# Optimization experiments

Measured on AMD Instinct MI355X. Metric: run time of the kernel, lower is better.

Reference implementation:

```python
import jax, jax.numpy as jnp
import numpy as np

N_EMBD = 1024
HEAD_SIZE = N_EMBD  # source bug: Block passes n_embd as head_size
EPS = 1e-5

def layernorm(x, g, b):
    mu = jnp.mean(x, axis=-1, keepdims=True)
    var = jnp.var(x, axis=-1, keepdims=True)
    return (x - mu) * jax.lax.rsqrt(var + EPS) * g + b

def setup_inputs() -> dict:
    key = jax.random.key(0)
    ks = jax.random.split(key, 8)
    B, T, C = 4, 2048, N_EMBD
    s = lambda fan_in: 1.0 / np.sqrt(fan_in)
    return {
        "x": jax.random.normal(ks[0], (B, T, C), dtype=jnp.float32),
        "Wk": jax.random.uniform(ks[1], (C, HEAD_SIZE), jnp.float32, -s(C), s(C)),
        "Wq": jax.random.uniform(ks[2], (C, HEAD_SIZE), jnp.float32, -s(C), s(C)),
        "Wv": jax.random.uniform(ks[3], (C, HEAD_SIZE), jnp.float32, -s(C), s(C)),
        "W1": jax.random.uniform(ks[4], (C, 4 * C), jnp.float32, -s(C), s(C)),
        "b1": jnp.zeros((4 * C,), jnp.float32),
        "W2": jax.random.uniform(ks[5], (4 * C, C), jnp.float32, -s(4 * C), s(4 * C)),
        "b2": jnp.zeros((C,), jnp.float32),
        "g1": jnp.ones((C,), jnp.float32),
        "be1": jnp.zeros((C,), jnp.float32),
        "g2": jnp.ones((C,), jnp.float32),
        "be2": jnp.zeros((C,), jnp.float32),
    }

def reference(x, Wk, Wq, Wv, W1, b1, W2, b2, g1, be1, g2, be2):
    B, T, C = x.shape
    h = layernorm(x, g1, be1)
    q = h @ Wq              # [B,T,H]
    k = h @ Wk
    v = h @ Wv
    wei = jnp.einsum('bth,bsh->bts', q, k) / jnp.sqrt(jnp.float32(C))
    causal = jnp.tril(jnp.ones((T, T), dtype=bool))
    wei = jnp.where(causal, wei, -jnp.inf)
    wei = jax.nn.softmax(wei, axis=-1)
    sa = jnp.einsum('bts,bsh->bth', wei, v)
    x = x + sa
    h2 = layernorm(x, g2, be2)
    ff = jax.nn.relu(h2 @ W1 + b1) @ W2 + b2
    return x + ff
```

## Files before the change

### kernel.cpp

```cpp
#include <hip/hip_runtime.h>
#include <hip/hip_bf16.h>


typedef __bf16 bf16x8_t __attribute__((ext_vector_type(8)));
typedef float f32x4_t __attribute__((ext_vector_type(4)));

__device__ __forceinline__ unsigned short f2bf(float f) {
    unsigned int u = __float_as_uint(f);
    u += 0x7fffu + ((u >> 16) & 1u);
    return (unsigned short)(u >> 16);
}
__device__ __forceinline__ float bf2f(unsigned short u) {
    return __uint_as_float((unsigned int)u << 16);
}

__device__ __forceinline__ void gload16(const void* g, void* lds) {
    __builtin_amdgcn_global_load_lds(
        (const __attribute__((address_space(1))) unsigned int*)g,
        (__attribute__((address_space(3))) unsigned int*)lds, 16, 0, 0);
}

#define SB0() __builtin_amdgcn_sched_barrier(0)
#define BAR() asm volatile("s_barrier" ::: "memory")
#define VM4_BAR() asm volatile("s_waitcnt vmcnt(4)\ns_barrier" ::: "memory")
#define VM0_BAR() asm volatile("s_waitcnt vmcnt(0)\ns_barrier" ::: "memory")

enum { EPI_F32 = 0, EPI_BF16 = 1, EPI_BIAS_RELU_BF16 = 2, EPI_RESID_F32 = 3,
       EPI_BIAS_RESID_F32 = 4 };

template <int EPI, bool CSKIP, bool KLIM>
__global__ __launch_bounds__(512, 2) void gemm256(
    const unsigned short* __restrict__ A,
    const unsigned short* __restrict__ Bm,
    void* __restrict__ Cout,
    const float* __restrict__ bias,
    const float* __restrict__ resid,
    int M, int N, int K, int lda, int ldb, float scale,
    long long batA, long long batB, long long batC, long long batR)
{
    __shared__ __align__(16) unsigned char lds[131072];

    const int gx = gridDim.x;
    const int nwg = gx * gridDim.y;
    int bl = blockIdx.y * gx + blockIdx.x;
    bl = (bl & 7) * (nwg >> 3) + (bl >> 3);
    const int bx = bl % gx, by = bl / gx;

    const int row0 = by * 256, col0 = bx * 256;
    if (CSKIP && col0 > row0) return;

    const int bz = blockIdx.z;
    const unsigned short* Ab = A + (long long)bz * batA + (long long)row0 * lda;
    const unsigned short* Bb = Bm + (long long)bz * batB + (long long)col0 * ldb;

    const int tid = threadIdx.x, lane = tid & 63, wid = tid >> 6;
    const int wrM = (wid >> 2) * 128;
    const int wcN = (wid & 3) * 64;
    const int lr = lane & 15, lg = lane >> 4;

    int Keff = K;
    if (KLIM) { int kl = row0 + 256; Keff = kl < K ? kl : K; }
    const int nkt = Keff >> 6;

    const int c0 = wid * 128 + lane;
    const int crow = c0 >> 2;
    const int sg = (c0 & 3) ^ ((c0 >> 4) & 3);
    const unsigned short* gA0 = Ab + (long long)crow * lda + sg * 8;
    const unsigned short* gA1 = gA0 + 16ll * lda;
    const unsigned short* gB0 = Bb + (long long)crow * ldb + sg * 8;
    const unsigned short* gB1 = gB0 + 16ll * ldb;

    const int sw = (lg ^ ((lr >> 2) & 3)) << 4;
    const int aoff = (wrM + lr) * 64 + sw;
    const int boff = 16384 + (wcN + lr) * 64 + sw;

    f32x4_t acc[8][4];
#pragma unroll
    for (int m = 0; m < 8; ++m)
#pragma unroll
        for (int n = 0; n < 4; ++n)
            acc[m][n] = (f32x4_t){0.f, 0.f, 0.f, 0.f};

    auto stageR = [&](int b, int r, int ktn) {
        const int kk = r >> 1, op = r & 1;
        const int ke = ktn * 64 + kk * 32;
        unsigned char* d = lds + b * 65536 + kk * 32768 + op * 16384 + wid * 2048;
        const unsigned short* g0 = (op ? gB0 : gA0) + ke;
        const unsigned short* g1 = (op ? gB1 : gA1) + ke;
        gload16(g0, d);
        gload16(g1, d + 1024);
    };

    bf16x8_t af[4], bv[4];
    auto dsA4 = [&](int b, int kk, int mq) {
        const unsigned char* u = lds + b * 65536 + kk * 32768;
#pragma unroll
        for (int j = 0; j < 4; ++j)
            af[j] = *(const bf16x8_t*)(u + aoff + (mq * 4 + j) * 1024);
    };
    auto dsB4 = [&](int b, int kk) {
        const unsigned char* u = lds + b * 65536 + kk * 32768;
#pragma unroll
        for (int n = 0; n < 4; ++n)
            bv[n] = *(const bf16x8_t*)(u + boff + n * 1024);
    };
    auto mf16 = [&](int mq) {
        __builtin_amdgcn_s_setprio(1);
#pragma unroll
        for (int j = 0; j < 4; ++j)
#pragma unroll
            for (int n = 0; n < 4; ++n)
                acc[mq * 4 + j][n] = __builtin_amdgcn_mfma_f32_16x16x32_bf16(
                    af[j], bv[n], acc[mq * 4 + j][n], 0, 0, 0);
        __builtin_amdgcn_s_setprio(0);
    };

    stageR(0, 0, 0); stageR(0, 1, 0); stageR(0, 2, 0); stageR(0, 3, 0);
    VM4_BAR();

    int kt = 0;
    for (; kt < nkt - 1; ++kt) {
        const int buf = kt & 1, nb = buf ^ 1;
        dsA4(buf, 0, 0); dsB4(buf, 0);
        stageR(nb, 0, kt + 1); stageR(nb, 1, kt + 1);
        BAR(); SB0();
        mf16(0); SB0();
        BAR();
        dsA4(buf, 0, 1);
        VM4_BAR(); SB0();
        mf16(1); SB0();
        BAR();
        dsA4(buf, 1, 0); dsB4(buf, 1);
        stageR(nb, 2, kt + 1); stageR(nb, 3, kt + 1);
        BAR(); SB0();
        mf16(0); SB0();
        BAR();
        dsA4(buf, 1, 1);
        VM4_BAR(); SB0();
        mf16(1); SB0();
        BAR();
    }
    {
        const int buf = kt & 1;
        dsA4(buf, 0, 0); dsB4(buf, 0);
        BAR(); SB0();
        mf16(0); SB0();
        BAR();
        dsA4(buf, 0, 1);
        VM0_BAR(); SB0();
        mf16(1); SB0();
        BAR();
        dsA4(buf, 1, 0); dsB4(buf, 1);
        BAR(); SB0();
        mf16(0); SB0();
        BAR();
        dsA4(buf, 1, 1);
        SB0();
        mf16(1); SB0();
    }

    const int ldc = N;
    float* Cf = (float*)Cout + (long long)bz * batC;
    unsigned short* Cb = (unsigned short*)Cout + (long long)bz * batC;
    const float* R = nullptr;
    if constexpr (EPI == EPI_RESID_F32 || EPI == EPI_BIAS_RESID_F32)
        R = resid + (long long)bz * batR;

#pragma unroll
    for (int m = 0; m < 8; ++m)
#pragma unroll
        for (int n = 0; n < 4; ++n)
#pragma unroll
            for (int j = 0; j < 4; ++j) {
                const int row = row0 + wrM + m * 16 + lg * 4 + j;
                const int col = col0 + wcN + n * 16 + lr;
                const long long idx = (long long)row * ldc + col;
                float v = acc[m][n][j] * scale;
                if constexpr (EPI == EPI_F32) {
                    Cf[idx] = v;
                } else if constexpr (EPI == EPI_BF16) {
                    Cb[idx] = f2bf(v);
                } else if constexpr (EPI == EPI_BIAS_RELU_BF16) {
                    v += bias[col];
                    v = v > 0.f ? v : 0.f;
                    Cb[idx] = f2bf(v);
                } else if constexpr (EPI == EPI_RESID_F32) {
                    Cf[idx] = v + R[idx];
                } else {
                    Cf[idx] = v + bias[col] + R[idx];
                }
            }
}

__global__ __launch_bounds__(256) void tconv_k(
    const float* __restrict__ in, unsigned short* __restrict__ out,
    int R, int Cc)
{
    __shared__ float t[64][65];
    const int r0 = blockIdx.y * 64, c0 = blockIdx.x * 64;
    const int tid = threadIdx.x;
    const int a = tid >> 4;
    const int b = tid & 15;
#pragma unroll
    for (int i = 0; i < 4; ++i) {
        const int row = a + i * 16;
        float4 v = *(const float4*)(in + (long long)(r0 + row) * Cc + c0 + b * 4);
        t[row][b * 4 + 0] = v.x; t[row][b * 4 + 1] = v.y;
        t[row][b * 4 + 2] = v.z; t[row][b * 4 + 3] = v.w;
    }
    __syncthreads();
#pragma unroll
    for (int i = 0; i < 4; ++i) {
        const int oc = a + i * 16;
        ushort4 o;
        o.x = f2bf(t[b * 4 + 0][oc]);
        o.y = f2bf(t[b * 4 + 1][oc]);
        o.z = f2bf(t[b * 4 + 2][oc]);
        o.w = f2bf(t[b * 4 + 3][oc]);
        *(ushort4*)(out + (long long)(c0 + oc) * R + r0 + b * 4) = o;
    }
}

__global__ __launch_bounds__(256) void vtrans_k(
    const unsigned short* __restrict__ in, unsigned short* __restrict__ out)
{
    __shared__ unsigned short t[64][72];
    const int r0 = blockIdx.x * 64;
    const int c0 = blockIdx.y * 64;
    const int tid = threadIdx.x;
#pragma unroll
    for (int i = 0; i < 2; ++i) {
        const int ch = tid * 2 + i;
        const int row = ch >> 3, cs = ch & 7;
        int4 v = *(const int4*)(in + (long long)(r0 + row) * 3072 + 2048 + c0 + cs * 8);
        *(int4*)&t[row][cs * 8] = v;
    }
    __syncthreads();
#pragma unroll
    for (int i = 0; i < 2; ++i) {
        const int w = tid * 2 + i;
        const int oc = w >> 3, orc = w & 7;
        unsigned short tmp[8];
#pragma unroll
        for (int j = 0; j < 8; ++j) tmp[j] = t[orc * 8 + j][oc];
        *(int4*)(out + (long long)(c0 + oc) * 8192 + r0 + orc * 8) = *(const int4*)tmp;
    }
}

__global__ __launch_bounds__(256) void ln_k(
    const float* __restrict__ x, const float* __restrict__ g,
    const float* __restrict__ be, unsigned short* __restrict__ out)
{
    const int wv = threadIdx.x >> 6, lane = threadIdx.x & 63;
    const long long row = blockIdx.x * 4 + wv;
    const float* xr = x + row * 1024;
    float4 v[4];
    float s = 0.f, q = 0.f;
#pragma unroll
    for (int j = 0; j < 4; ++j) {
        v[j] = *(const float4*)(xr + j * 256 + lane * 4);
        s += v[j].x + v[j].y + v[j].z + v[j].w;
        q += v[j].x * v[j].x + v[j].y * v[j].y + v[j].z * v[j].z + v[j].w * v[j].w;
    }
#pragma unroll
    for (int off = 32; off > 0; off >>= 1) {
        s += __shfl_xor(s, off);
        q += __shfl_xor(q, off);
    }
    const float mean = s * (1.0f / 1024.0f);
    const float var  = q * (1.0f / 1024.0f) - mean * mean;
    const float rstd = rsqrtf(var + 1e-5f);
#pragma unroll
    for (int j = 0; j < 4; ++j) {
        float4 gv = *(const float4*)(g + j * 256 + lane * 4);
        float4 bv = *(const float4*)(be + j * 256 + lane * 4);
        ushort4 o;
        o.x = f2bf((v[j].x - mean) * rstd * gv.x + bv.x);
        o.y = f2bf((v[j].y - mean) * rstd * gv.y + bv.y);
        o.z = f2bf((v[j].z - mean) * rstd * gv.z + bv.z);
        o.w = f2bf((v[j].w - mean) * rstd * gv.w + bv.w);
        *(ushort4*)(out + row * 1024 + j * 256 + lane * 4) = o;
    }
}

__global__ __launch_bounds__(256) void softmax_k(
    const unsigned short* __restrict__ S, unsigned short* __restrict__ P, int T)
{
    __shared__ float rowl[2048];
    __shared__ float sred[4];
    const int t = blockIdx.x;
    const long long base = ((long long)blockIdx.y * T + t) * (long long)T;
    const unsigned short* srow = S + base;
    unsigned short* prow = P + base;
    const int n = t + 1;
    const int lim = ((t >> 8) + 1) << 8;
    const int tid = threadIdx.x;

    const int n8 = n >> 3;
    for (int i = tid; i < n8; i += 256) {
        int4 r = ((const int4*)srow)[i];
        const unsigned short* u = (const unsigned short*)&r;
#pragma unroll
        for (int j = 0; j < 8; ++j) rowl[i * 8 + j] = bf2f(u[j]);
    }
    for (int i = (n8 << 3) + tid; i < n; i += 256) rowl[i] = bf2f(srow[i]);
    __syncthreads();

    float mx = -3.0e38f;
    for (int i = tid; i < n; i += 256) mx = fmaxf(mx, rowl[i]);
#pragma unroll
    for (int off = 32; off > 0; off >>= 1) mx = fmaxf(mx, __shfl_xor(mx, off));
    if ((tid & 63) == 0) sred[tid >> 6] = mx;
    __syncthreads();
    mx = fmaxf(fmaxf(sred[0], sred[1]), fmaxf(sred[2], sred[3]));
    __syncthreads();

    float sum = 0.f;
    for (int i = tid; i < n; i += 256) {
        float e = __expf(rowl[i] - mx);
        rowl[i] = e;
        sum += e;
    }
#pragma unroll
    for (int off = 32; off > 0; off >>= 1) sum += __shfl_xor(sum, off);
    if ((tid & 63) == 0) sred[tid >> 6] = sum;
    __syncthreads();
    sum = sred[0] + sred[1] + sred[2] + sred[3];
    const float inv = 1.0f / sum;

    for (int i = tid; i < n; i += 256) prow[i] = f2bf(rowl[i] * inv);
    for (int i = n + tid; i < lim; i += 256) prow[i] = 0;
}

__global__ __launch_bounds__(256) void ffadd_k(
    const float4* __restrict__ p0, const float4* __restrict__ p1,
    const float4* __restrict__ xr, const float4* __restrict__ b2,
    float4* __restrict__ out, int n4)
{
    int i = blockIdx.x * 256 + threadIdx.x;
    const int stride = gridDim.x * 256;
    for (; i < n4; i += stride) {
        float4 a = p0[i], b = p1[i], c = xr[i], d = b2[i & 255];
        float4 o;
        o.x = a.x + b.x + c.x + d.x;
        o.y = a.y + b.y + c.y + d.y;
        o.z = a.z + b.z + c.z + d.z;
        o.w = a.w + b.w + c.w + d.w;
        out[i] = o;
    }
}

extern "C" void kernel_launch(void* const* d_in, const int* in_sizes, int n_in,
                              void* d_out, int out_size, void* d_ws, size_t ws_size,
                              hipStream_t stream)
{
    const int B = 4, T = 2048, C = 1024, F = 4096;
    const float* x   = (const float*)d_in[0];
    const float* Wk  = (const float*)d_in[1];
    const float* Wq  = (const float*)d_in[2];
    const float* Wv  = (const float*)d_in[3];
    const float* W1  = (const float*)d_in[4];
    const float* b1  = (const float*)d_in[5];
    const float* W2  = (const float*)d_in[6];
    const float* b2  = (const float*)d_in[7];
    const float* g1  = (const float*)d_in[8];
    const float* be1 = (const float*)d_in[9];
    const float* g2  = (const float*)d_in[10];
    const float* be2 = (const float*)d_in[11];

    char* ws = (char*)d_ws;
    const size_t MB = 1ull << 20;
    unsigned short* h     = (unsigned short*)(ws + 0);
    unsigned short* qkv   = (unsigned short*)(ws + 16 * MB);
    unsigned short* vT    = (unsigned short*)(ws + 64 * MB);
    float*          pbuf  = (float*)(ws + 16 * MB);
    float*          xres  = (float*)(ws + 80 * MB);
    unsigned short* S     = (unsigned short*)(ws + 112 * MB);
    unsigned short* P     = (unsigned short*)(ws + 144 * MB);
    unsigned short* ff1   = (unsigned short*)(ws + 112 * MB);
    unsigned short* wqkvT = (unsigned short*)(ws + 176 * MB);
    unsigned short* w1T   = (unsigned short*)(ws + 182 * MB);
    unsigned short* w2T   = (unsigned short*)(ws + 190 * MB);

    tconv_k<<<dim3(16, 16), 256, 0, stream>>>(Wq, wqkvT, C, C);
    tconv_k<<<dim3(16, 16), 256, 0, stream>>>(Wk, wqkvT + C * C, C, C);
    tconv_k<<<dim3(16, 16), 256, 0, stream>>>(Wv, wqkvT + 2 * C * C, C, C);
    tconv_k<<<dim3(64, 16), 256, 0, stream>>>(W1, w1T, C, F);
    tconv_k<<<dim3(16, 64), 256, 0, stream>>>(W2, w2T, F, C);

    ln_k<<<dim3(B * T / 4), 256, 0, stream>>>(x, g1, be1, h);

    dim3 gqkv(3 * C / 256, (B * T) / 256, 1);
    gemm256<EPI_BF16, false, false><<<gqkv, 512, 0, stream>>>(
        h, wqkvT, qkv, nullptr, nullptr, B * T, 3 * C, C, C, C, 1.0f, 0, 0, 0, 0);

    vtrans_k<<<dim3(B * T / 64, C / 64), 256, 0, stream>>>(qkv, vT);

    dim3 gsc(T / 256, T / 256, B);
    gemm256<EPI_BF16, true, false><<<gsc, 512, 0, stream>>>(
        qkv, qkv + C, S, nullptr, nullptr, T, T, C, 3 * C, 3 * C, 0.03125f,
        (long long)T * 3 * C, (long long)T * 3 * C, (long long)T * T, 0);

    softmax_k<<<dim3(T, B), 256, 0, stream>>>(S, P, T);

    dim3 gsa(C / 256, T / 256, B);
    gemm256<EPI_RESID_F32, false, true><<<gsa, 512, 0, stream>>>(
        P, vT, xres, nullptr, x, T, C, T, T, B * T, 1.0f,
        (long long)T * T, (long long)T, (long long)T * C, (long long)T * C);

    ln_k<<<dim3(B * T / 4), 256, 0, stream>>>(xres, g2, be2, h);

    dim3 gf1(F / 256, (B * T) / 256, 1);
    gemm256<EPI_BIAS_RELU_BF16, false, false><<<gf1, 512, 0, stream>>>(
        h, w1T, ff1, b1, nullptr, B * T, F, C, C, C, 1.0f, 0, 0, 0, 0);

    dim3 gf2(C / 256, (B * T) / 256, 2);
    gemm256<EPI_F32, false, false><<<gf2, 512, 0, stream>>>(
        ff1, w2T, pbuf, nullptr, nullptr, B * T, C, F / 2, F, F, 1.0f,
        (long long)(F / 2), (long long)(F / 2), (long long)(B * T) * C, 0);

    ffadd_k<<<dim3(2048), 256, 0, stream>>>(
        (const float4*)pbuf, (const float4*)(pbuf + (long long)(B * T) * C),
        (const float4*)xres, (const float4*)b2, (float4*)d_out,
        (B * T) * C / 4);
}
```

Measured before the change: 406.7 us.

## Merge GEMM K-loop phases and change LDS swizzle pattern

Restructures the 256x256 bf16 GEMM main loop from four half-width MFMA phases per K-tile to two full 32-MFMA phases, each loading all 8 A fragments and 4 B fragments at once and issuing A and B global-to-LDS copies together. It also changes the XOR swizzle on both the global-load side and the LDS-read side to use different row bits, aiming to reduce LDS bank conflicts. Fewer barriers per tile cut synchronization overhead, at the cost of more live fragment registers and coarser overlap between loads and MFMAs.

```diff
diff --git a/kernel.cpp b/kernel.cpp
--- a/kernel.cpp
+++ b/kernel.cpp
@@ -64,13 +64,13 @@
 
     const int c0 = wid * 128 + lane;
     const int crow = c0 >> 2;
-    const int sg = (c0 & 3) ^ ((c0 >> 4) & 3);
+    const int sg = (c0 & 3) ^ ((c0 >> 3) & 3);
     const unsigned short* gA0 = Ab + (long long)crow * lda + sg * 8;
     const unsigned short* gA1 = gA0 + 16ll * lda;
     const unsigned short* gB0 = Bb + (long long)crow * ldb + sg * 8;
     const unsigned short* gB1 = gB0 + 16ll * ldb;
 
-    const int sw = (lg ^ ((lr >> 2) & 3)) << 4;
+    const int sw = (lg ^ ((lr >> 1) & 3)) << 4;
     const int aoff = (wrM + lr) * 64 + sw;
     const int boff = 16384 + (wcN + lr) * 64 + sw;
 
@@ -81,82 +81,63 @@
         for (int n = 0; n < 4; ++n)
             acc[m][n] = (f32x4_t){0.f, 0.f, 0.f, 0.f};
 
-    auto stageR = [&](int b, int r, int ktn) {
-        const int kk = r >> 1, op = r & 1;
+    auto stage2 = [&](int b, int kk, int ktn) {
         const int ke = ktn * 64 + kk * 32;
-        unsigned char* d = lds + b * 65536 + kk * 32768 + op * 16384 + wid * 2048;
-        const unsigned short* g0 = (op ? gB0 : gA0) + ke;
-        const unsigned short* g1 = (op ? gB1 : gA1) + ke;
-        gload16(g0, d);
-        gload16(g1, d + 1024);
+        unsigned char* uA = lds + b * 65536 + kk * 32768 + wid * 2048;
+        unsigned char* uB = uA + 16384;
+        gload16(gA0 + ke, uA);
+        gload16(gA1 + ke, uA + 1024);
+        gload16(gB0 + ke, uB);
+        gload16(gB1 + ke, uB + 1024);
     };
 
-    bf16x8_t af[4], bv[4];
-    auto dsA4 = [&](int b, int kk, int mq) {
+    bf16x8_t af[8], bv[4];
+    auto dsAB = [&](int b, int kk) {
         const unsigned char* u = lds + b * 65536 + kk * 32768;
 #pragma unroll
-        for (int j = 0; j < 4; ++j)
-            af[j] = *(const bf16x8_t*)(u + aoff + (mq * 4 + j) * 1024);
-    };
-    auto dsB4 = [&](int b, int kk) {
-        const unsigned char* u = lds + b * 65536 + kk * 32768;
+        for (int m = 0; m < 8; ++m)
+            af[m] = *(const bf16x8_t*)(u + aoff + m * 1024);
 #pragma unroll
         for (int n = 0; n < 4; ++n)
             bv[n] = *(const bf16x8_t*)(u + boff + n * 1024);
     };
-    auto mf16 = [&](int mq) {
+    auto mf32 = [&]() {
         __builtin_amdgcn_s_setprio(1);
 #pragma unroll
-        for (int j = 0; j < 4; ++j)
+        for (int m = 0; m < 8; ++m)
 #pragma unroll
             for (int n = 0; n < 4; ++n)
-                acc[mq * 4 + j][n] = __builtin_amdgcn_mfma_f32_16x16x32_bf16(
-                    af[j], bv[n], acc[mq * 4 + j][n], 0, 0, 0);
+                acc[m][n] = __builtin_amdgcn_mfma_f32_16x16x32_bf16(
+                    af[m], bv[n], acc[m][n], 0, 0, 0);
         __builtin_amdgcn_s_setprio(0);
     };
 
-    stageR(0, 0, 0); stageR(0, 1, 0); stageR(0, 2, 0); stageR(0, 3, 0);
+    stage2(0, 0, 0); stage2(0, 1, 0);
     VM4_BAR();
 
     int kt = 0;
     for (; kt < nkt - 1; ++kt) {
         const int buf = kt & 1, nb = buf ^ 1;
-        dsA4(buf, 0, 0); dsB4(buf, 0);
-        stageR(nb, 0, kt + 1); stageR(nb, 1, kt + 1);
+        dsAB(buf, 0);
+        stage2(nb, 0, kt + 1);
         BAR(); SB0();
-        mf16(0); SB0();
-        BAR();
-        dsA4(buf, 0, 1);
-        VM4_BAR(); SB0();
-        mf16(1); SB0();
-        BAR();
-        dsA4(buf, 1, 0); dsB4(buf, 1);
-        stageR(nb, 2, kt + 1); stageR(nb, 3, kt + 1);
+        mf32(); SB0();
+        VM4_BAR();
+        dsAB(buf, 1);
+        stage2(nb, 1, kt + 1);
         BAR(); SB0();
-        mf16(0); SB0();
-        BAR();
-        dsA4(buf, 1, 1);
-        VM4_BAR(); SB0();
-        mf16(1); SB0();
-        BAR();
+        mf32(); SB0();
+        VM4_BAR();
     }
     {
         const int buf = kt & 1;
-        dsA4(buf, 0, 0); dsB4(buf, 0);
+        dsAB(buf, 0);
         BAR(); SB0();
-        mf16(0); SB0();
-        BAR();
-        dsA4(buf, 0, 1);
-        VM0_BAR(); SB0();
-        mf16(1); SB0();
-        BAR();
-        dsA4(buf, 1, 0); dsB4(buf, 1);
+        mf32(); SB0();
+        VM0_BAR();
+        dsAB(buf, 1);
         BAR(); SB0();
-        mf16(0); SB0();
-        BAR();
-        dsA4(buf, 1, 1);
-        SB0();
-        mf16(1); SB0();
+        mf32(); SB0();
     }
 
     const int ldc = N;
```

Result: faster. 390.8 us (-3.9%).
